# Kernel tuning notes

Hardware: AMD Instinct MI355X
Metric: run time of the kernel (lower is better)

The kernel has to match this reference:

```python
import jax, jax.numpy as jnp
import numpy as np

ALIGN_WEIGHT = 1.0
UNIFORM_WEIGHT = 1.0
ALIGN_ALPHA = 2.0
UNIFORM_T = 2.0
EPS = 1e-12  # F.normalize eps


def setup_inputs() -> dict:
    key = jax.random.key(0)
    ka, kb = jax.random.split(key)
    B, D = 4096, 256
    return {
        "embeddings_a": jax.random.normal(ka, (B, D), dtype=jnp.float32),
        "embeddings_b": jax.random.normal(kb, (B, D), dtype=jnp.float32),
    }


def _l2_normalize(x):
    # matches F.normalize(p=2, dim=1): x / max(||x||, eps)
    n = jnp.sqrt(jnp.sum(x * x, axis=1, keepdims=True))
    return x / jnp.maximum(n, EPS)


def reference(embeddings_a, embeddings_b):
    a = _l2_normalize(embeddings_a)
    b = _l2_normalize(embeddings_b)

    # alignment: mean ||a_i - b_i||^alpha (alpha=2 -> squared euclidean)
    diff = a - b
    dist = jnp.sqrt(jnp.sum(diff * diff, axis=1))
    align_loss = jnp.mean(dist ** ALIGN_ALPHA)

    # uniformity over concatenated views: mean over strict upper triangle of
    # exp(-t * d_ij^2). Matrix is symmetric with exp(0)=1 on the diagonal, so
    # mean_{i<j} = (sum_all - n) / (n*(n-1)). d^2 = 2 - 2<x_i, x_j> on sphere.
    x = jnp.concatenate([a, b], axis=0)  # [n, d]
    n = x.shape[0]
    gram = x @ x.T                        # [n, n]
    sq = jnp.sum(x * x, axis=1)           # [n]
    d2 = jnp.maximum(sq[:, None] + sq[None, :] - 2.0 * gram, 0.0)
    e = jnp.exp(-UNIFORM_T * d2)
    uniform_loss = (jnp.sum(e) - n) / (n * (n - 1))

    return ALIGN_WEIGHT * align_loss + UNIFORM_WEIGHT * uniform_loss
```

## Files before the change

### kernel.cpp

```cpp
#include <hip/hip_runtime.h>
#include <math.h>

#define D_DIM 256

typedef __attribute__((ext_vector_type(8))) short short8v;
typedef __attribute__((ext_vector_type(16))) float f32x16;

#define AS_GLOBAL(p) ((const __attribute__((address_space(1))) void*)(p))
#define AS_LDS(p)    ((__attribute__((address_space(3))) void*)(p))

__device__ __forceinline__ unsigned short f2bf(float f) {
    unsigned int u = __float_as_uint(f);
    unsigned int r = (u + 0x7fffu + ((u >> 16) & 1u)) >> 16;
    return (unsigned short)r;
}

__global__ __launch_bounds__(256) void normalize_kernel(
        const float* __restrict__ A, const float* __restrict__ Bm,
        unsigned short* __restrict__ Xb, float* __restrict__ SQ,
        float* __restrict__ partials, int B_rows) {
    __shared__ float red[4];
    int lane = threadIdx.x & 63;
    int w    = threadIdx.x >> 6;
    int i    = blockIdx.x * 4 + w;

    const float4* A4 = (const float4*)(A + (size_t)i * D_DIM);
    const float4* B4 = (const float4*)(Bm + (size_t)i * D_DIM);
    float4 av = A4[lane];
    float4 bv = B4[lane];

    float sa = av.x*av.x + av.y*av.y + av.z*av.z + av.w*av.w;
    float sb = bv.x*bv.x + bv.y*bv.y + bv.z*bv.z + bv.w*bv.w;
    #pragma unroll
    for (int off = 32; off > 0; off >>= 1) {
        sa += __shfl_xor(sa, off, 64);
        sb += __shfl_xor(sb, off, 64);
    }
    float dena = fmaxf(sqrtf(sa), 1e-12f);
    float denb = fmaxf(sqrtf(sb), 1e-12f);
    float ia = 1.0f / dena, ib = 1.0f / denb;

    float4 an = {av.x*ia, av.y*ia, av.z*ia, av.w*ia};
    float4 bn = {bv.x*ib, bv.y*ib, bv.z*ib, bv.w*ib};

    ushort4 ua = {f2bf(an.x), f2bf(an.y), f2bf(an.z), f2bf(an.w)};
    ushort4 ub = {f2bf(bn.x), f2bf(bn.y), f2bf(bn.z), f2bf(bn.w)};
    ((ushort4*)(Xb + (size_t)i * D_DIM))[lane]            = ua;
    ((ushort4*)(Xb + (size_t)(B_rows + i) * D_DIM))[lane] = ub;

    float dx = an.x-bn.x, dy = an.y-bn.y, dz = an.z-bn.z, dw = an.w-bn.w;
    float sd = dx*dx + dy*dy + dz*dz + dw*dw;
    #pragma unroll
    for (int off = 32; off > 0; off >>= 1) sd += __shfl_down(sd, off, 64);

    if (lane == 0) {
        SQ[i]          = sa * ia * ia;
        SQ[B_rows + i] = sb * ib * ib;
        red[w] = sd;
    }
    __syncthreads();
    if (threadIdx.x == 0)
        atomicAdd(&partials[blockIdx.x & 63], red[0]+red[1]+red[2]+red[3]);
}

__device__ __forceinline__ short8v frag_read(const unsigned short* base, int r, int kb) {
    int off = r * 128 + (kb ^ ((r & 7) << 4));
    return *reinterpret_cast<const short8v*>(reinterpret_cast<const char*>(base) + off);
}

__global__ __launch_bounds__(256) void uniform_mfma_kernel(
        const unsigned short* __restrict__ Xb, const float* __restrict__ SQ,
        float* __restrict__ partials) {
    int ib = blockIdx.x, jb = blockIdx.y;
    if (jb < ib) return;

    __shared__ __align__(16) unsigned short As[128 * 64];
    __shared__ __align__(16) unsigned short Bs[128 * 64];
    __shared__ float sqa[128], sqb[128], red[4];

    int t    = threadIdx.x;
    int lane = t & 63;
    int w    = t >> 6;
    int wr   = w >> 1, wc = w & 1;

    int rowA0 = ib * 128, rowB0 = jb * 128;
    if (t < 128) sqa[t] = SQ[rowA0 + t];
    else         sqb[t - 128] = SQ[rowB0 + t - 128];

    f32x16 acc[2][2] = {};

    int r_a0 = wr * 64 + (lane & 31), r_a1 = r_a0 + 32;
    int r_b0 = wc * 64 + (lane & 31), r_b1 = r_b0 + 32;

    for (int k0 = 0; k0 < D_DIM; k0 += 64) {
        __syncthreads();
        #pragma unroll
        for (int it = 0; it < 4; ++it) {
            int row   = w * 32 + it * 8 + (lane >> 3);
            int chunk = ((lane & 7) ^ ((lane >> 3) & 7)) << 3;
            const unsigned short* srcA = Xb + (size_t)(rowA0 + row) * D_DIM + k0 + chunk;
            const unsigned short* srcB = Xb + (size_t)(rowB0 + row) * D_DIM + k0 + chunk;
            unsigned short* dA = As + (w * 32 + it * 8) * 64;
            unsigned short* dB = Bs + (w * 32 + it * 8) * 64;
            __builtin_amdgcn_global_load_lds(AS_GLOBAL(srcA), AS_LDS(dA), 16, 0, 0);
            __builtin_amdgcn_global_load_lds(AS_GLOBAL(srcB), AS_LDS(dB), 16, 0, 0);
        }
        __syncthreads();

        #pragma unroll
        for (int kk = 0; kk < 4; ++kk) {
            int kb = kk * 32 + ((lane >> 5) << 4);
            short8v a0 = frag_read(As, r_a0, kb);
            short8v a1 = frag_read(As, r_a1, kb);
            short8v b0 = frag_read(Bs, r_b0, kb);
            short8v b1 = frag_read(Bs, r_b1, kb);
            acc[0][0] = __builtin_amdgcn_mfma_f32_32x32x16_bf16(a0, b0, acc[0][0], 0, 0, 0);
            acc[0][1] = __builtin_amdgcn_mfma_f32_32x32x16_bf16(a0, b1, acc[0][1], 0, 0, 0);
            acc[1][0] = __builtin_amdgcn_mfma_f32_32x32x16_bf16(a1, b0, acc[1][0], 0, 0, 0);
            acc[1][1] = __builtin_amdgcn_mfma_f32_32x32x16_bf16(a1, b1, acc[1][1], 0, 0, 0);
        }
    }

    float s = 0.0f;
    int col = lane & 31;
    int rhi = (lane >> 5) * 4;
    #pragma unroll
    for (int si = 0; si < 2; ++si)
        #pragma unroll
        for (int sj = 0; sj < 2; ++sj)
            #pragma unroll
            for (int reg = 0; reg < 16; ++reg) {
                int il = wr * 64 + si * 32 + (reg & 3) + 8 * (reg >> 2) + rhi;
                int jl = wc * 64 + sj * 32 + col;
                float d2 = fmaxf(sqa[il] + sqb[jl] - 2.0f * acc[si][sj][reg], 0.0f);
                s += __expf(-2.0f * d2);
            }
    if (ib != jb) s *= 2.0f;

    #pragma unroll
    for (int off = 32; off > 0; off >>= 1) s += __shfl_down(s, off, 64);
    if (lane == 0) red[w] = s;
    __syncthreads();
    if (t == 0)
        atomicAdd(&partials[64 + ((ib * 7 + jb * 13) & 63)], red[0]+red[1]+red[2]+red[3]);
}

__global__ void finalize_kernel(const float* __restrict__ partials,
                                float* __restrict__ out, int B_rows) {
    int t = threadIdx.x;
    float al = partials[t];
    float un = partials[64 + t];
    #pragma unroll
    for (int off = 32; off > 0; off >>= 1) {
        al += __shfl_down(al, off, 64);
        un += __shfl_down(un, off, 64);
    }
    if (t == 0) {
        float n = (float)(2 * B_rows);
        out[0] = al / (float)B_rows + (un - n) / (n * (n - 1.0f));
    }
}

extern "C" void kernel_launch(void* const* d_in, const int* in_sizes, int n_in,
                              void* d_out, int out_size, void* d_ws, size_t ws_size,
                              hipStream_t stream) {
    const float* A  = (const float*)d_in[0];
    const float* Bm = (const float*)d_in[1];
    float* out = (float*)d_out;

    int B_rows = in_sizes[0] / D_DIM;
    int n_tot  = 2 * B_rows;

    unsigned short* Xb = (unsigned short*)d_ws;
    float* SQ       = (float*)(Xb + (size_t)n_tot * D_DIM);
    float* partials = SQ + n_tot;

    hipMemsetAsync(partials, 0, 128 * sizeof(float), stream);

    normalize_kernel<<<B_rows / 4, 256, 0, stream>>>(A, Bm, Xb, SQ, partials, B_rows);

    int nb = n_tot / 128;
    uniform_mfma_kernel<<<dim3(nb, nb), 256, 0, stream>>>(Xb, SQ, partials);

    finalize_kernel<<<1, 64, 0, stream>>>(partials, out, B_rows);
}
```

Baseline: 98.38 us.

## Use 256x256 triangular tiles with double-buffered LDS pipeline for Gram exp-sum

Result: slower. 104.7 us (+6.4%).

```diff
diff --git a/kernel.cpp b/kernel.cpp
--- a/kernel.cpp
+++ b/kernel.cpp
@@ -2,8 +2,10 @@
 #include <math.h>
 
 #define D_DIM 256
-
-typedef __attribute__((ext_vector_type(8))) short short8v;
+#define TILE  256
+#define BK    64
+
+typedef __attribute__((ext_vector_type(8)))  short short8v;
 typedef __attribute__((ext_vector_type(16))) float f32x16;
 
 #define AS_GLOBAL(p) ((const __attribute__((address_space(1))) void*)(p))
@@ -68,70 +70,107 @@
     return *reinterpret_cast<const short8v*>(reinterpret_cast<const char*>(base) + off);
 }
 
-__global__ __launch_bounds__(256) void uniform_mfma_kernel(
+__global__ __launch_bounds__(512, 2) void uniform_mfma_kernel(
         const unsigned short* __restrict__ Xb, const float* __restrict__ SQ,
-        float* __restrict__ partials) {
-    int ib = blockIdx.x, jb = blockIdx.y;
-    if (jb < ib) return;
-
-    __shared__ __align__(16) unsigned short As[128 * 64];
-    __shared__ __align__(16) unsigned short Bs[128 * 64];
-    __shared__ float sqa[128], sqb[128], red[4];
+        float* __restrict__ partials, int n_panels) {
+    __shared__ __align__(16) unsigned short As[2][TILE * BK];
+    __shared__ __align__(16) unsigned short Bs[2][TILE * BK];
+    __shared__ float sqa[TILE], sqb[TILE], red[8];
 
     int t    = threadIdx.x;
     int lane = t & 63;
     int w    = t >> 6;
-    int wr   = w >> 1, wc = w & 1;
-
-    int rowA0 = ib * 128, rowB0 = jb * 128;
-    if (t < 128) sqa[t] = SQ[rowA0 + t];
-    else         sqb[t - 128] = SQ[rowB0 + t - 128];
-
-    f32x16 acc[2][2] = {};
+    int wr   = w >> 1;
+    int wc   = w & 1;
+
+    int rem = blockIdx.x;
+    int ib  = 0;
+    while (rem >= n_panels - ib) { rem -= n_panels - ib; ++ib; }
+    int jb = ib + rem;
+
+    int rowA0 = ib * TILE, rowB0 = jb * TILE;
+    if (t < TILE) sqa[t]        = SQ[rowA0 + t];
+    else          sqb[t - TILE] = SQ[rowB0 + t - TILE];
+
+#define STAGE(bi, k0)                                                         \
+    do {                                                                      \
+        _Pragma("unroll")                                                     \
+        for (int it = 0; it < 4; ++it) {                                      \
+            int row   = w * 32 + it * 8 + (lane >> 3);                        \
+            int chunk = ((lane & 7) ^ ((lane >> 3) & 7)) << 3;                \
+            const unsigned short* sA = Xb + (size_t)(rowA0 + row) * D_DIM + (k0) + chunk; \
+            const unsigned short* sB = Xb + (size_t)(rowB0 + row) * D_DIM + (k0) + chunk; \
+            unsigned short* dA = &As[bi][(w * 32 + it * 8) * BK];             \
+            unsigned short* dB = &Bs[bi][(w * 32 + it * 8) * BK];             \
+            __builtin_amdgcn_global_load_lds(AS_GLOBAL(sA), AS_LDS(dA), 16, 0, 0); \
+            __builtin_amdgcn_global_load_lds(AS_GLOBAL(sB), AS_LDS(dB), 16, 0, 0); \
+        }                                                                     \
+    } while (0)
+
+    f32x16 acc[2][4] = {};
 
     int r_a0 = wr * 64 + (lane & 31), r_a1 = r_a0 + 32;
-    int r_b0 = wc * 64 + (lane & 31), r_b1 = r_b0 + 32;
-
-    for (int k0 = 0; k0 < D_DIM; k0 += 64) {
-        __syncthreads();
-        #pragma unroll
-        for (int it = 0; it < 4; ++it) {
-            int row   = w * 32 + it * 8 + (lane >> 3);
-            int chunk = ((lane & 7) ^ ((lane >> 3) & 7)) << 3;
-            const unsigned short* srcA = Xb + (size_t)(rowA0 + row) * D_DIM + k0 + chunk;
-            const unsigned short* srcB = Xb + (size_t)(rowB0 + row) * D_DIM + k0 + chunk;
-            unsigned short* dA = As + (w * 32 + it * 8) * 64;
-            unsigned short* dB = Bs + (w * 32 + it * 8) * 64;
-            __builtin_amdgcn_global_load_lds(AS_GLOBAL(srcA), AS_LDS(dA), 16, 0, 0);
-            __builtin_amdgcn_global_load_lds(AS_GLOBAL(srcB), AS_LDS(dB), 16, 0, 0);
-        }
-        __syncthreads();
-
-        #pragma unroll
-        for (int kk = 0; kk < 4; ++kk) {
-            int kb = kk * 32 + ((lane >> 5) << 4);
-            short8v a0 = frag_read(As, r_a0, kb);
-            short8v a1 = frag_read(As, r_a1, kb);
-            short8v b0 = frag_read(Bs, r_b0, kb);
-            short8v b1 = frag_read(Bs, r_b1, kb);
-            acc[0][0] = __builtin_amdgcn_mfma_f32_32x32x16_bf16(a0, b0, acc[0][0], 0, 0, 0);
-            acc[0][1] = __builtin_amdgcn_mfma_f32_32x32x16_bf16(a0, b1, acc[0][1], 0, 0, 0);
-            acc[1][0] = __builtin_amdgcn_mfma_f32_32x32x16_bf16(a1, b0, acc[1][0], 0, 0, 0);
-            acc[1][1] = __builtin_amdgcn_mfma_f32_32x32x16_bf16(a1, b1, acc[1][1], 0, 0, 0);
-        }
-    }
-
-    float s = 0.0f;
-    int col = lane & 31;
-    int rhi = (lane >> 5) * 4;
+    int r_b0 = wc * 128 + (lane & 31);
+    int r_b1 = r_b0 + 32, r_b2 = r_b0 + 64, r_b3 = r_b0 + 96;
+
+#define COMPUTE(bi)                                                           \
+    do {                                                                      \
+        _Pragma("unroll")                                                     \
+        for (int kk = 0; kk < 4; ++kk) {                                      \
+            int kb = kk * 32 + ((lane >> 5) << 4);                            \
+            short8v a0 = frag_read(&As[bi][0], r_a0, kb);                     \
+            short8v a1 = frag_read(&As[bi][0], r_a1, kb);                     \
+            short8v b0 = frag_read(&Bs[bi][0], r_b0, kb);                     \
+            short8v b1 = frag_read(&Bs[bi][0], r_b1, kb);                     \
+            short8v b2 = frag_read(&Bs[bi][0], r_b2, kb);                     \
+            short8v b3 = frag_read(&Bs[bi][0], r_b3, kb);                     \
+            acc[0][0] = __builtin_amdgcn_mfma_f32_32x32x16_bf16(a0, b0, acc[0][0], 0, 0, 0); \
+            acc[0][1] = __builtin_amdgcn_mfma_f32_32x32x16_bf16(a0, b1, acc[0][1], 0, 0, 0); \
+            acc[0][2] = __builtin_amdgcn_mfma_f32_32x32x16_bf16(a0, b2, acc[0][2], 0, 0, 0); \
+            acc[0][3] = __builtin_amdgcn_mfma_f32_32x32x16_bf16(a0, b3, acc[0][3], 0, 0, 0); \
+            acc[1][0] = __builtin_amdgcn_mfma_f32_32x32x16_bf16(a1, b0, acc[1][0], 0, 0, 0); \
+            acc[1][1] = __builtin_amdgcn_mfma_f32_32x32x16_bf16(a1, b1, acc[1][1], 0, 0, 0); \
+            acc[1][2] = __builtin_amdgcn_mfma_f32_32x32x16_bf16(a1, b2, acc[1][2], 0, 0, 0); \
+            acc[1][3] = __builtin_amdgcn_mfma_f32_32x32x16_bf16(a1, b3, acc[1][3], 0, 0, 0); \
+        }                                                                     \
+    } while (0)
+
+#define PIPE_FENCE()                                                          \
+    do {                                                                      \
+        asm volatile("s_waitcnt vmcnt(0)" ::: "memory");                      \
+        __builtin_amdgcn_s_barrier();                                         \
+        __builtin_amdgcn_sched_barrier(0);                                    \
+    } while (0)
+
+    STAGE(0, 0);
+    asm volatile("s_waitcnt vmcnt(0)" ::: "memory");
+    __syncthreads();
+
+    STAGE(1, 64);
+    COMPUTE(0);
+    PIPE_FENCE();
+
+    STAGE(0, 128);
+    COMPUTE(1);
+    PIPE_FENCE();
+
+    STAGE(1, 192);
+    COMPUTE(0);
+    PIPE_FENCE();
+
+    COMPUTE(1);
+
+    float s   = 0.0f;
+    int   col = lane & 31;
+    int   rhi = (lane >> 5) * 4;
     #pragma unroll
     for (int si = 0; si < 2; ++si)
         #pragma unroll
-        for (int sj = 0; sj < 2; ++sj)
+        for (int sj = 0; sj < 4; ++sj)
             #pragma unroll
             for (int reg = 0; reg < 16; ++reg) {
                 int il = wr * 64 + si * 32 + (reg & 3) + 8 * (reg >> 2) + rhi;
-                int jl = wc * 64 + sj * 32 + col;
+                int jl = wc * 128 + sj * 32 + col;
                 float d2 = fmaxf(sqa[il] + sqb[jl] - 2.0f * acc[si][sj][reg], 0.0f);
                 s += __expf(-2.0f * d2);
             }
@@ -141,8 +180,13 @@
     for (int off = 32; off > 0; off >>= 1) s += __shfl_down(s, off, 64);
     if (lane == 0) red[w] = s;
     __syncthreads();
-    if (t == 0)
-        atomicAdd(&partials[64 + ((ib * 7 + jb * 13) & 63)], red[0]+red[1]+red[2]+red[3]);
+    if (t == 0) {
+        float tot = red[0]+red[1]+red[2]+red[3]+red[4]+red[5]+red[6]+red[7];
+        atomicAdd(&partials[64 + (blockIdx.x & 63)], tot);
+    }
+#undef STAGE
+#undef COMPUTE
+#undef PIPE_FENCE
 }
 
 __global__ void finalize_kernel(const float* __restrict__ partials,
@@ -179,8 +223,9 @@
 
     normalize_kernel<<<B_rows / 4, 256, 0, stream>>>(A, Bm, Xb, SQ, partials, B_rows);
 
-    int nb = n_tot / 128;
-    uniform_mfma_kernel<<<dim3(nb, nb), 256, 0, stream>>>(Xb, SQ, partials);
+    int n_panels = n_tot / TILE;
+    int n_blocks = n_panels * (n_panels + 1) / 2;
+    uniform_mfma_kernel<<<n_blocks, 512, 0, stream>>>(Xb, SQ, partials, n_panels);
 
     finalize_kernel<<<1, 64, 0, stream>>>(partials, out, B_rows);
 }
```
